# Performance work log

Measured on AMD Instinct MI355X. Metric: run time of the kernel, lower is better.

## Reference

```python
import jax, jax.numpy as jnp
import numpy as np

HIDDEN = 2048
NUM_EXPERTS = 64
TOP_K = 2


def setup_inputs() -> dict:
    key = jax.random.key(0)
    k1, k2 = jax.random.split(key)
    x = jax.random.normal(k1, (4, 4096, HIDDEN), dtype=jnp.float32)
    # nn.Linear(hidden, num_experts, bias=False): weight shape [E, H], y = x @ W.T
    W = jax.random.normal(k2, (NUM_EXPERTS, HIDDEN), dtype=jnp.float32) * (HIDDEN ** -0.5)
    return {"x": x, "W": W}


def reference(x, W):
    B, S, H = x.shape
    E, K = NUM_EXPERTS, TOP_K
    xf = x.reshape(-1, H)                       # [N, H]
    gate_logits = xf @ W.T                      # [N, E]
    routing_probs = jax.nn.softmax(gate_logits, axis=-1)
    top_k_probs, top_k_indices = jax.lax.top_k(routing_probs, K)  # [N, K]
    denom = jnp.sum(top_k_probs, axis=-1, keepdims=True) + 1e-6
    routing_weights = (top_k_probs / denom).reshape(B, S, K)
    expert_indices = top_k_indices.reshape(B, S, K)

    # aux load-balancing loss (training path)
    N = xf.shape[0]
    # expert_mask.mean(0): fraction of tokens assigned to each expert
    assign_per_expert = jnp.zeros((E,), jnp.float32).at[top_k_indices.reshape(-1)].add(1.0) / N
    prob_per_expert = jnp.mean(routing_probs, axis=0)             # [E]
    aux_loss = (jnp.sum(prob_per_expert * prob_per_expert) * E
                + jnp.sum(assign_per_expert * assign_per_expert) * E)

    # expert_counts update (bincount over selected indices)
    expert_counts = jnp.zeros((E,), jnp.float32).at[top_k_indices.reshape(-1)].add(1.0)

    return routing_weights, expert_indices, aux_loss, expert_counts
```

## Files before the change

kernel.cpp:

```cpp
#include <hip/hip_runtime.h>

#define HID 2048
#define NEXP 64
#define NTOK 16384
#define TM 32
#define NTHREADS 256
#define NBLK (NTOK / TM)
#define NCHUNK 32
#define KPH 4
#define CPW 8
#define CHUNK_B 24576
#define WS_W_OFF 262144

#define OUT_IDX_OFF (2 * NTOK)
#define OUT_AUX_OFF (4 * NTOK)
#define OUT_CNT_OFF (4 * NTOK + 1)

typedef __attribute__((ext_vector_type(8))) short bhalf8;
typedef __attribute__((ext_vector_type(16))) float f32x16;

__device__ __forceinline__ void split3(float v, unsigned short& h1, unsigned short& h2, unsigned short& h3) {
    unsigned int u = __float_as_uint(v);
    unsigned int r1 = (u + 0x7FFFu + ((u >> 16) & 1u)) & 0xFFFF0000u;
    float f1 = __uint_as_float(r1);
    float d1 = v - f1;
    unsigned int u2 = __float_as_uint(d1);
    unsigned int r2 = (u2 + 0x7FFFu + ((u2 >> 16) & 1u)) & 0xFFFF0000u;
    float f2 = __uint_as_float(r2);
    float d2 = d1 - f2;
    h1 = (unsigned short)(r1 >> 16);
    h2 = (unsigned short)(r2 >> 16);
    h3 = (unsigned short)(__float_as_uint(d2) >> 16);
}

__device__ __forceinline__ void xsplit(float4 va, float4 vb, bhalf8& o1, bhalf8& o2, bhalf8& o3) {
    float f[8] = {va.x, va.y, va.z, va.w, vb.x, vb.y, vb.z, vb.w};
    union U { bhalf8 v; unsigned int u[4]; } u1, u2, u3;
#pragma unroll
    for (int t = 0; t < 4; t++) {
        float a = f[2 * t], b = f[2 * t + 1];
        unsigned int ua = __float_as_uint(a), ub = __float_as_uint(b);
        float da = a - __uint_as_float(ua & 0xFFFF0000u);
        float db = b - __uint_as_float(ub & 0xFFFF0000u);
        unsigned int uda = __float_as_uint(da), udb = __float_as_uint(db);
        float da2 = da - __uint_as_float(uda & 0xFFFF0000u);
        float db2 = db - __uint_as_float(udb & 0xFFFF0000u);
        u1.u[t] = (ua >> 16) | (ub & 0xFFFF0000u);
        u2.u[t] = (uda >> 16) | (udb & 0xFFFF0000u);
        u3.u[t] = (__float_as_uint(da2) >> 16) | (__float_as_uint(db2) & 0xFFFF0000u);
    }
    o1 = u1.v; o2 = u2.v; o3 = u3.v;
}

__global__ __launch_bounds__(256) void wsplit_kernel(const float* __restrict__ W,
                                                     char* __restrict__ wq) {
    int idx8 = (blockIdx.x * 256 + threadIdx.x) * 8;
    int e = idx8 >> 11;
    int k0 = idx8 & 2047;
    int c = k0 >> 6, ks = (k0 >> 4) & 3, half = (k0 >> 3) & 1;
    int g = e >> 5, l = (e & 31) + 32 * half;
    const float4* wp = (const float4*)(W + (size_t)e * HID + k0);
    float4 v0 = wp[0], v1 = wp[1];
    float f[8] = {v0.x, v0.y, v0.z, v0.w, v1.x, v1.y, v1.z, v1.w};
    unsigned int p1[4], p2[4], p3[4];
#pragma unroll
    for (int t = 0; t < 4; t++) {
        unsigned short a1, a2, a3, b1, b2, b3;
        split3(f[2 * t], a1, a2, a3);
        split3(f[2 * t + 1], b1, b2, b3);
        p1[t] = (unsigned int)a1 | ((unsigned int)b1 << 16);
        p2[t] = (unsigned int)a2 | ((unsigned int)b2 << 16);
        p3[t] = (unsigned int)a3 | ((unsigned int)b3 << 16);
    }
    char* base = wq + (size_t)(((c * 4 + ks) * 3 + 0) * 2 + g) * 1024 + l * 16;
    *(uint4*)(base)        = make_uint4(p1[0], p1[1], p1[2], p1[3]);
    *(uint4*)(base + 2048) = make_uint4(p2[0], p2[1], p2[2], p2[3]);
    *(uint4*)(base + 4096) = make_uint4(p3[0], p3[1], p3[2], p3[3]);
}

__device__ __forceinline__ void load_chunk(const float* xc, float4 (&pa)[4], float4 (&pb)[4]) {
#pragma unroll
    for (int ks = 0; ks < 4; ks++) {
        pa[ks] = *(const float4*)(xc + ks * 16);
        pb[ks] = *(const float4*)(xc + ks * 16 + 4);
    }
}

__device__ __forceinline__ void compute_chunk(const float4 (&pa)[4], const float4 (&pb)[4],
                                              const char* wc, f32x16& acc0, f32x16& acc1) {
#pragma unroll
    for (int ks = 0; ks < 4; ks++) {
        bhalf8 A1, A2, A3;
        xsplit(pa[ks], pb[ks], A1, A2, A3);
        const char* wk = wc + ks * 6144;
        bhalf8 B1 = *(const bhalf8*)(wk);
        bhalf8 B2 = *(const bhalf8*)(wk + 2048);
        bhalf8 B3 = *(const bhalf8*)(wk + 4096);
        acc0 = __builtin_amdgcn_mfma_f32_32x32x16_bf16(A1, B1, acc0, 0, 0, 0);
        acc0 = __builtin_amdgcn_mfma_f32_32x32x16_bf16(A1, B2, acc0, 0, 0, 0);
        acc0 = __builtin_amdgcn_mfma_f32_32x32x16_bf16(A2, B1, acc0, 0, 0, 0);
        acc0 = __builtin_amdgcn_mfma_f32_32x32x16_bf16(A1, B3, acc0, 0, 0, 0);
        acc0 = __builtin_amdgcn_mfma_f32_32x32x16_bf16(A2, B2, acc0, 0, 0, 0);
        acc0 = __builtin_amdgcn_mfma_f32_32x32x16_bf16(A3, B1, acc0, 0, 0, 0);
        bhalf8 C1 = *(const bhalf8*)(wk + 1024);
        bhalf8 C2 = *(const bhalf8*)(wk + 2048 + 1024);
        bhalf8 C3 = *(const bhalf8*)(wk + 4096 + 1024);
        acc1 = __builtin_amdgcn_mfma_f32_32x32x16_bf16(A1, C1, acc1, 0, 0, 0);
        acc1 = __builtin_amdgcn_mfma_f32_32x32x16_bf16(A1, C2, acc1, 0, 0, 0);
        acc1 = __builtin_amdgcn_mfma_f32_32x32x16_bf16(A2, C1, acc1, 0, 0, 0);
        acc1 = __builtin_amdgcn_mfma_f32_32x32x16_bf16(A1, C3, acc1, 0, 0, 0);
        acc1 = __builtin_amdgcn_mfma_f32_32x32x16_bf16(A2, C2, acc1, 0, 0, 0);
        acc1 = __builtin_amdgcn_mfma_f32_32x32x16_bf16(A3, C1, acc1, 0, 0, 0);
    }
}

__global__ __launch_bounds__(NTHREADS, 2) void router_main(
    const float* __restrict__ x, const char* __restrict__ wq,
    float* __restrict__ out, float* __restrict__ partials)
{
    __shared__ float slab[KPH * TM * 68];
    __shared__ float smax[TM];
    __shared__ float sinvZ[TM];
    __shared__ float scount[NEXP];
    __shared__ float sprob[NEXP];

    const int tid = threadIdx.x;
    const int w = tid >> 6;
    const int lane = tid & 63;
    const int r = lane & 31;
    const int h = lane >> 5;
    const int n0 = blockIdx.x * TM;

    const float* xrow = x + (size_t)(n0 + r) * HID + h * 8;

    f32x16 acc0, acc1;
#pragma unroll
    for (int i = 0; i < 16; i++) { acc0[i] = 0.f; acc1[i] = 0.f; }

    float4 pa0[4], pb0[4], pa1[4], pb1[4];
    const float* xbase = xrow + (w * CPW) * 64;
    load_chunk(xbase, pa0, pb0);
    const char* wcbase = wq + (size_t)(w * CPW) * CHUNK_B + lane * 16;

#pragma unroll 1
    for (int i = 0; i < CPW; i += 2) {
        if (i + 1 < CPW) load_chunk(xbase + (i + 1) * 64, pa1, pb1);
        compute_chunk(pa0, pb0, wcbase + (size_t)i * CHUNK_B, acc0, acc1);
        if (i + 2 < CPW) load_chunk(xbase + (i + 2) * 64, pa0, pb0);
        if (i + 1 < CPW) compute_chunk(pa1, pb1, wcbase + (size_t)(i + 1) * CHUNK_B, acc0, acc1);
    }

#pragma unroll
    for (int reg = 0; reg < 16; reg++) {
        int row = (reg & 3) + 8 * (reg >> 2) + 4 * h;
        slab[(w * TM + row) * 68 + r]      = acc0[reg];
        slab[(w * TM + row) * 68 + 32 + r] = acc1[reg];
    }
    if (tid < NEXP) { scount[tid] = 0.f; sprob[tid] = 0.f; }
    __syncthreads();

    float* logits = slab;
#pragma unroll
    for (int idx = tid; idx < TM * NEXP; idx += NTHREADS) {
        int t = idx >> 6, e = idx & 63;
        logits[t * 68 + e] = slab[(0 * TM + t) * 68 + e] + slab[(1 * TM + t) * 68 + e]
                           + slab[(2 * TM + t) * 68 + e] + slab[(3 * TM + t) * 68 + e];
    }
    __syncthreads();

    if (tid < TM) {
        const int t = tid;
        float m1 = -3.4e38f, m2 = -3.4e38f;
        int i1 = 0, i2 = 0;
        for (int e = 0; e < NEXP; e++) {
            float v = logits[t * 68 + e];
            if (v > m1) { m2 = m1; i2 = i1; m1 = v; i1 = e; }
            else if (v > m2) { m2 = v; i2 = e; }
        }
        float Z = 0.f;
        for (int e = 0; e < NEXP; e++)
            Z += __expf(logits[t * 68 + e] - m1);
        float invZ = 1.f / Z;
        float p1 = invZ;
        float p2 = __expf(m2 - m1) * invZ;
        float denom = p1 + p2 + 1e-6f;
        int n = n0 + t;
        out[2 * n + 0] = p1 / denom;
        out[2 * n + 1] = p2 / denom;
        out[OUT_IDX_OFF + 2 * n + 0] = (float)i1;
        out[OUT_IDX_OFF + 2 * n + 1] = (float)i2;
        smax[t] = m1;
        sinvZ[t] = invZ;
        atomicAdd(&scount[i1], 1.f);
        atomicAdd(&scount[i2], 1.f);
    }
    __syncthreads();

    {
        const int e = tid & 63, tq = tid >> 6;
        float s = 0.f;
#pragma unroll
        for (int j = 0; j < 8; j++) {
            int t = tq * 8 + j;
            s += __expf(logits[t * 68 + e] - smax[t]) * sinvZ[t];
        }
        atomicAdd(&sprob[e], s);
    }
    __syncthreads();

    if (tid < NEXP) {
        partials[blockIdx.x * 128 + tid]      = sprob[tid];
        partials[blockIdx.x * 128 + 64 + tid] = scount[tid];
    }
}

__global__ __launch_bounds__(128) void router_finish(const float* __restrict__ partials,
                                                     float* __restrict__ out)
{
    __shared__ float red[2];
    const int t = threadIdx.x;
    float s = 0.f;
#pragma unroll 8
    for (int b = 0; b < NBLK; b++)
        s += partials[b * 128 + t];
    const float invN = 1.f / (float)NTOK;
    if (t >= 64) out[OUT_CNT_OFF + (t - 64)] = s;
    float sc = s * invN;
    float v = sc * sc;
#pragma unroll
    for (int off = 32; off > 0; off >>= 1)
        v += __shfl_down(v, off);
    if ((t & 63) == 0) red[t >> 6] = v;
    __syncthreads();
    if (t == 0) out[OUT_AUX_OFF] = (red[0] + red[1]) * (float)NEXP;
}

extern "C" void kernel_launch(void* const* d_in, const int* in_sizes, int n_in,
                              void* d_out, int out_size, void* d_ws, size_t ws_size,
                              hipStream_t stream)
{
    const float* x = (const float*)d_in[0];
    const float* W = (const float*)d_in[1];
    float* out = (float*)d_out;
    float* partials = (float*)d_ws;
    char* wq = (char*)d_ws + WS_W_OFF;

    wsplit_kernel<<<64, 256, 0, stream>>>(W, wq);
    router_main<<<NBLK, NTHREADS, 0, stream>>>(x, wq, out, partials);
    router_finish<<<1, 128, 0, stream>>>(partials, out);
}
```

Baseline: 229.9 us.

## Split router GEMM across token and expert tiles with 16x16 MFMA

Replaces the K-split work division, where each of 4 waves covered a quarter of the hidden dimension over all 32 tokens and 64 experts, with an output-tile split. Each of 8 waves now owns 16 tokens by 16 experts over the full hidden dimension, using 16x16x32 bf16 MFMA and a matching new weight layout. This removes the cross-wave slab reduction in shared memory and doubles the threads per block. The finish kernel also spreads the partial reduction over 1024 threads. The cost is that x rows are now read by four waves each, so global or cache traffic for x rises.

Measured after the change: 262.3 us. +14.1%, slower.

```diff
diff --git a/kernel.cpp b/kernel.cpp
--- a/kernel.cpp
+++ b/kernel.cpp
@@ -4,12 +4,9 @@
 #define NEXP 64
 #define NTOK 16384
 #define TM 32
-#define NTHREADS 256
+#define NTHREADS 512
 #define NBLK (NTOK / TM)
-#define NCHUNK 32
-#define KPH 4
-#define CPW 8
-#define CHUNK_B 24576
+#define NKS 64
 #define WS_W_OFF 262144
 
 #define OUT_IDX_OFF (2 * NTOK)
@@ -17,7 +14,7 @@
 #define OUT_CNT_OFF (4 * NTOK + 1)
 
 typedef __attribute__((ext_vector_type(8))) short bhalf8;
-typedef __attribute__((ext_vector_type(16))) float f32x16;
+typedef __attribute__((ext_vector_type(4))) float f32x4;
 
 __device__ __forceinline__ void split3(float v, unsigned short& h1, unsigned short& h2, unsigned short& h3) {
     unsigned int u = __float_as_uint(v);
@@ -57,8 +54,8 @@
     int idx8 = (blockIdx.x * 256 + threadIdx.x) * 8;
     int e = idx8 >> 11;
     int k0 = idx8 & 2047;
-    int c = k0 >> 6, ks = (k0 >> 4) & 3, half = (k0 >> 3) & 1;
-    int g = e >> 5, l = (e & 31) + 32 * half;
+    int ks = k0 >> 5, q = (k0 >> 3) & 3;
+    int eh = e >> 4, lane = q * 16 + (e & 15);
     const float4* wp = (const float4*)(W + (size_t)e * HID + k0);
     float4 v0 = wp[0], v1 = wp[1];
     float f[8] = {v0.x, v0.y, v0.z, v0.w, v1.x, v1.y, v1.z, v1.w};
@@ -72,53 +69,31 @@
         p2[t] = (unsigned int)a2 | ((unsigned int)b2 << 16);
         p3[t] = (unsigned int)a3 | ((unsigned int)b3 << 16);
     }
-    char* base = wq + (size_t)(((c * 4 + ks) * 3 + 0) * 2 + g) * 1024 + l * 16;
+    char* base = wq + (size_t)((ks * 3 + 0) * 4 + eh) * 1024 + lane * 16;
     *(uint4*)(base)        = make_uint4(p1[0], p1[1], p1[2], p1[3]);
-    *(uint4*)(base + 2048) = make_uint4(p2[0], p2[1], p2[2], p2[3]);
-    *(uint4*)(base + 4096) = make_uint4(p3[0], p3[1], p3[2], p3[3]);
-}
-
-__device__ __forceinline__ void load_chunk(const float* xc, float4 (&pa)[4], float4 (&pb)[4]) {
-#pragma unroll
-    for (int ks = 0; ks < 4; ks++) {
-        pa[ks] = *(const float4*)(xc + ks * 16);
-        pb[ks] = *(const float4*)(xc + ks * 16 + 4);
-    }
-}
-
-__device__ __forceinline__ void compute_chunk(const float4 (&pa)[4], const float4 (&pb)[4],
-                                              const char* wc, f32x16& acc0, f32x16& acc1) {
-#pragma unroll
-    for (int ks = 0; ks < 4; ks++) {
-        bhalf8 A1, A2, A3;
-        xsplit(pa[ks], pb[ks], A1, A2, A3);
-        const char* wk = wc + ks * 6144;
-        bhalf8 B1 = *(const bhalf8*)(wk);
-        bhalf8 B2 = *(const bhalf8*)(wk + 2048);
-        bhalf8 B3 = *(const bhalf8*)(wk + 4096);
-        acc0 = __builtin_amdgcn_mfma_f32_32x32x16_bf16(A1, B1, acc0, 0, 0, 0);
-        acc0 = __builtin_amdgcn_mfma_f32_32x32x16_bf16(A1, B2, acc0, 0, 0, 0);
-        acc0 = __builtin_amdgcn_mfma_f32_32x32x16_bf16(A2, B1, acc0, 0, 0, 0);
-        acc0 = __builtin_amdgcn_mfma_f32_32x32x16_bf16(A1, B3, acc0, 0, 0, 0);
-        acc0 = __builtin_amdgcn_mfma_f32_32x32x16_bf16(A2, B2, acc0, 0, 0, 0);
-        acc0 = __builtin_amdgcn_mfma_f32_32x32x16_bf16(A3, B1, acc0, 0, 0, 0);
-        bhalf8 C1 = *(const bhalf8*)(wk + 1024);
-        bhalf8 C2 = *(const bhalf8*)(wk + 2048 + 1024);
-        bhalf8 C3 = *(const bhalf8*)(wk + 4096 + 1024);
-        acc1 = __builtin_amdgcn_mfma_f32_32x32x16_bf16(A1, C1, acc1, 0, 0, 0);
-        acc1 = __builtin_amdgcn_mfma_f32_32x32x16_bf16(A1, C2, acc1, 0, 0, 0);
-        acc1 = __builtin_amdgcn_mfma_f32_32x32x16_bf16(A2, C1, acc1, 0, 0, 0);
-        acc1 = __builtin_amdgcn_mfma_f32_32x32x16_bf16(A1, C3, acc1, 0, 0, 0);
-        acc1 = __builtin_amdgcn_mfma_f32_32x32x16_bf16(A2, C2, acc1, 0, 0, 0);
-        acc1 = __builtin_amdgcn_mfma_f32_32x32x16_bf16(A3, C1, acc1, 0, 0, 0);
-    }
-}
-
-__global__ __launch_bounds__(NTHREADS, 2) void router_main(
+    *(uint4*)(base + 4096) = make_uint4(p2[0], p2[1], p2[2], p2[3]);
+    *(uint4*)(base + 8192) = make_uint4(p3[0], p3[1], p3[2], p3[3]);
+}
+
+__device__ __forceinline__ void kstep6(float4 xa, float4 xb, const char* wk, f32x4& acc) {
+    bhalf8 A1, A2, A3;
+    xsplit(xa, xb, A1, A2, A3);
+    bhalf8 B1 = *(const bhalf8*)(wk);
+    bhalf8 B2 = *(const bhalf8*)(wk + 4096);
+    bhalf8 B3 = *(const bhalf8*)(wk + 8192);
+    acc = __builtin_amdgcn_mfma_f32_16x16x32_bf16(A1, B1, acc, 0, 0, 0);
+    acc = __builtin_amdgcn_mfma_f32_16x16x32_bf16(A1, B2, acc, 0, 0, 0);
+    acc = __builtin_amdgcn_mfma_f32_16x16x32_bf16(A2, B1, acc, 0, 0, 0);
+    acc = __builtin_amdgcn_mfma_f32_16x16x32_bf16(A1, B3, acc, 0, 0, 0);
+    acc = __builtin_amdgcn_mfma_f32_16x16x32_bf16(A2, B2, acc, 0, 0, 0);
+    acc = __builtin_amdgcn_mfma_f32_16x16x32_bf16(A3, B1, acc, 0, 0, 0);
+}
+
+__global__ __launch_bounds__(NTHREADS, 4) void router_main(
     const float* __restrict__ x, const char* __restrict__ wq,
     float* __restrict__ out, float* __restrict__ partials)
 {
-    __shared__ float slab[KPH * TM * 68];
+    __shared__ float logits[TM * 68];
     __shared__ float smax[TM];
     __shared__ float sinvZ[TM];
     __shared__ float scount[NEXP];
@@ -127,45 +102,41 @@
     const int tid = threadIdx.x;
     const int w = tid >> 6;
     const int lane = tid & 63;
-    const int r = lane & 31;
-    const int h = lane >> 5;
+    const int th = w >> 2;
+    const int eh = w & 3;
+    const int m = lane & 15;
+    const int q = lane >> 4;
     const int n0 = blockIdx.x * TM;
 
-    const float* xrow = x + (size_t)(n0 + r) * HID + h * 8;
-
-    f32x16 acc0, acc1;
-#pragma unroll
-    for (int i = 0; i < 16; i++) { acc0[i] = 0.f; acc1[i] = 0.f; }
-
-    float4 pa0[4], pb0[4], pa1[4], pb1[4];
-    const float* xbase = xrow + (w * CPW) * 64;
-    load_chunk(xbase, pa0, pb0);
-    const char* wcbase = wq + (size_t)(w * CPW) * CHUNK_B + lane * 16;
+    const float* xrow = x + (size_t)(n0 + th * 16 + m) * HID + q * 8;
+    const char* wbase = wq + (size_t)eh * 1024 + lane * 16;
+
+    f32x4 accA = {0.f, 0.f, 0.f, 0.f}, accB = {0.f, 0.f, 0.f, 0.f};
+
+    float4 xa0 = *(const float4*)(xrow);
+    float4 xb0 = *(const float4*)(xrow + 4);
+    float4 xa1 = *(const float4*)(xrow + 32);
+    float4 xb1 = *(const float4*)(xrow + 36);
 
 #pragma unroll 1
-    for (int i = 0; i < CPW; i += 2) {
-        if (i + 1 < CPW) load_chunk(xbase + (i + 1) * 64, pa1, pb1);
-        compute_chunk(pa0, pb0, wcbase + (size_t)i * CHUNK_B, acc0, acc1);
-        if (i + 2 < CPW) load_chunk(xbase + (i + 2) * 64, pa0, pb0);
-        if (i + 1 < CPW) compute_chunk(pa1, pb1, wcbase + (size_t)(i + 1) * CHUNK_B, acc0, acc1);
-    }
-
-#pragma unroll
-    for (int reg = 0; reg < 16; reg++) {
-        int row = (reg & 3) + 8 * (reg >> 2) + 4 * h;
-        slab[(w * TM + row) * 68 + r]      = acc0[reg];
-        slab[(w * TM + row) * 68 + 32 + r] = acc1[reg];
-    }
+    for (int ks = 0; ks < NKS; ks += 2) {
+        float4 ya, yb, za, zb;
+        if (ks + 2 < NKS) {
+            const float* xn = xrow + (ks + 2) * 32;
+            ya = *(const float4*)(xn);
+            yb = *(const float4*)(xn + 4);
+            za = *(const float4*)(xn + 32);
+            zb = *(const float4*)(xn + 36);
+        }
+        kstep6(xa0, xb0, wbase + (size_t)ks * 12288, accA);
+        kstep6(xa1, xb1, wbase + (size_t)(ks + 1) * 12288, accB);
+        xa0 = ya; xb0 = yb; xa1 = za; xb1 = zb;
+    }
+
+#pragma unroll
+    for (int r = 0; r < 4; r++)
+        logits[(th * 16 + q * 4 + r) * 68 + eh * 16 + m] = accA[r] + accB[r];
     if (tid < NEXP) { scount[tid] = 0.f; sprob[tid] = 0.f; }
-    __syncthreads();
-
-    float* logits = slab;
-#pragma unroll
-    for (int idx = tid; idx < TM * NEXP; idx += NTHREADS) {
-        int t = idx >> 6, e = idx & 63;
-        logits[t * 68 + e] = slab[(0 * TM + t) * 68 + e] + slab[(1 * TM + t) * 68 + e]
-                           + slab[(2 * TM + t) * 68 + e] + slab[(3 * TM + t) * 68 + e];
-    }
     __syncthreads();
 
     if (tid < TM) {
@@ -200,8 +171,8 @@
         const int e = tid & 63, tq = tid >> 6;
         float s = 0.f;
 #pragma unroll
-        for (int j = 0; j < 8; j++) {
-            int t = tq * 8 + j;
+        for (int j = 0; j < 4; j++) {
+            int t = tq * 4 + j;
             s += __expf(logits[t * 68 + e] - smax[t]) * sinvZ[t];
         }
         atomicAdd(&sprob[e], s);
@@ -214,25 +185,33 @@
     }
 }
 
-__global__ __launch_bounds__(128) void router_finish(const float* __restrict__ partials,
-                                                     float* __restrict__ out)
+__global__ __launch_bounds__(1024) void router_finish(const float* __restrict__ partials,
+                                                      float* __restrict__ out)
 {
+    __shared__ float sred[8 * 128];
     __shared__ float red[2];
-    const int t = threadIdx.x;
+    const int t = threadIdx.x & 127;
+    const int g = threadIdx.x >> 7;
     float s = 0.f;
 #pragma unroll 8
-    for (int b = 0; b < NBLK; b++)
-        s += partials[b * 128 + t];
-    const float invN = 1.f / (float)NTOK;
-    if (t >= 64) out[OUT_CNT_OFF + (t - 64)] = s;
-    float sc = s * invN;
-    float v = sc * sc;
-#pragma unroll
-    for (int off = 32; off > 0; off >>= 1)
-        v += __shfl_down(v, off);
-    if ((t & 63) == 0) red[t >> 6] = v;
-    __syncthreads();
-    if (t == 0) out[OUT_AUX_OFF] = (red[0] + red[1]) * (float)NEXP;
+    for (int i = 0; i < 64; i++)
+        s += partials[(g * 64 + i) * 128 + t];
+    sred[g * 128 + t] = s;
+    __syncthreads();
+    if (threadIdx.x < 128) {
+        float tot = 0.f;
+#pragma unroll
+        for (int gg = 0; gg < 8; gg++) tot += sred[gg * 128 + t];
+        if (t >= 64) out[OUT_CNT_OFF + (t - 64)] = tot;
+        float sc = tot * (1.f / (float)NTOK);
+        float v = sc * sc;
+#pragma unroll
+        for (int off = 32; off > 0; off >>= 1)
+            v += __shfl_down(v, off);
+        if ((t & 63) == 0) red[t >> 6] = v;
+    }
+    __syncthreads();
+    if (threadIdx.x == 0) out[OUT_AUX_OFF] = (red[0] + red[1]) * (float)NEXP;
 }
 
 extern "C" void kernel_launch(void* const* d_in, const int* in_sizes, int n_in,
@@ -247,5 +226,5 @@
 
     wsplit_kernel<<<64, 256, 0, stream>>>(W, wq);
     router_main<<<NBLK, NTHREADS, 0, stream>>>(x, wq, out, partials);
-    router_finish<<<1, 128, 0, stream>>>(partials, out);
-}
+    router_finish<<<1, 1024, 0, stream>>>(partials, out);
+}
```

## Double waves per block, rotate chunk order across blocks, parallelize final reduction

Applied to the files above, without the earlier changes.

The main kernel now runs 8 waves per 512-thread block, splitting the hidden dimension into 8 partial sums of 4 chunks each instead of 4 waves with 8 chunks each. Chunk order is rotated by block index so concurrent blocks read different parts of the weight buffer, and the unrolled-by-two prefetch is replaced by a single-step prefetch with register copies. The finish kernel uses 1024 threads to reduce the 512 block partials in 8 parallel groups, which shortens its serial loop. The costs are larger slab shared memory (8x32x68 floats), higher occupancy demands from the launch bounds (4 blocks of 512 threads), and possible register pressure.

New measurement: 243.7 us. 6.0% more time.

```diff
diff --git a/kernel.cpp b/kernel.cpp
--- a/kernel.cpp
+++ b/kernel.cpp
@@ -4,11 +4,11 @@
 #define NEXP 64
 #define NTOK 16384
 #define TM 32
-#define NTHREADS 256
+#define NTHREADS 512
 #define NBLK (NTOK / TM)
 #define NCHUNK 32
-#define KPH 4
-#define CPW 8
+#define KPH 8
+#define CPW 4
 #define CHUNK_B 24576
 #define WS_W_OFF 262144
 
@@ -114,7 +114,7 @@
     }
 }
 
-__global__ __launch_bounds__(NTHREADS, 2) void router_main(
+__global__ __launch_bounds__(NTHREADS, 4) void router_main(
     const float* __restrict__ x, const char* __restrict__ wq,
     float* __restrict__ out, float* __restrict__ partials)
 {
@@ -130,6 +130,7 @@
     const int r = lane & 31;
     const int h = lane >> 5;
     const int n0 = blockIdx.x * TM;
+    const int brot = blockIdx.x & 3;
 
     const float* xrow = x + (size_t)(n0 + r) * HID + h * 8;
 
@@ -138,16 +139,17 @@
     for (int i = 0; i < 16; i++) { acc0[i] = 0.f; acc1[i] = 0.f; }
 
     float4 pa0[4], pb0[4], pa1[4], pb1[4];
-    const float* xbase = xrow + (w * CPW) * 64;
-    load_chunk(xbase, pa0, pb0);
-    const char* wcbase = wq + (size_t)(w * CPW) * CHUNK_B + lane * 16;
+    int c0 = w + 8 * brot;
+    load_chunk(xrow + c0 * 64, pa0, pb0);
 
 #pragma unroll 1
-    for (int i = 0; i < CPW; i += 2) {
-        if (i + 1 < CPW) load_chunk(xbase + (i + 1) * 64, pa1, pb1);
-        compute_chunk(pa0, pb0, wcbase + (size_t)i * CHUNK_B, acc0, acc1);
-        if (i + 2 < CPW) load_chunk(xbase + (i + 2) * 64, pa0, pb0);
-        if (i + 1 < CPW) compute_chunk(pa1, pb1, wcbase + (size_t)(i + 1) * CHUNK_B, acc0, acc1);
+    for (int i = 0; i < CPW; i++) {
+        int cn = w + 8 * ((i + 1 + brot) & 3);
+        if (i + 1 < CPW) load_chunk(xrow + cn * 64, pa1, pb1);
+        int c = w + 8 * ((i + brot) & 3);
+        compute_chunk(pa0, pb0, wq + (size_t)c * CHUNK_B + lane * 16, acc0, acc1);
+#pragma unroll
+        for (int ks = 0; ks < 4; ks++) { pa0[ks] = pa1[ks]; pb0[ks] = pb1[ks]; }
     }
 
 #pragma unroll
@@ -163,8 +165,10 @@
 #pragma unroll
     for (int idx = tid; idx < TM * NEXP; idx += NTHREADS) {
         int t = idx >> 6, e = idx & 63;
-        logits[t * 68 + e] = slab[(0 * TM + t) * 68 + e] + slab[(1 * TM + t) * 68 + e]
-                           + slab[(2 * TM + t) * 68 + e] + slab[(3 * TM + t) * 68 + e];
+        float v = 0.f;
+#pragma unroll
+        for (int p = 0; p < KPH; p++) v += slab[(p * TM + t) * 68 + e];
+        logits[t * 68 + e] = v;
     }
     __syncthreads();
 
@@ -200,39 +204,47 @@
         const int e = tid & 63, tq = tid >> 6;
         float s = 0.f;
 #pragma unroll
-        for (int j = 0; j < 8; j++) {
-            int t = tq * 8 + j;
+        for (int j = 0; j < 4; j++) {
+            int t = tq * 4 + j;
             s += __expf(logits[t * 68 + e] - smax[t]) * sinvZ[t];
         }
         atomicAdd(&sprob[e], s);
     }
     __syncthreads();
 
-    if (tid < NEXP) {
-        partials[blockIdx.x * 128 + tid]      = sprob[tid];
-        partials[blockIdx.x * 128 + 64 + tid] = scount[tid];
-    }
-}
-
-__global__ __launch_bounds__(128) void router_finish(const float* __restrict__ partials,
-                                                     float* __restrict__ out)
+    if (tid < 128) {
+        float v = (tid < 64) ? sprob[tid] : scount[tid - 64];
+        partials[blockIdx.x * 128 + tid] = v;
+    }
+}
+
+__global__ __launch_bounds__(1024) void router_finish(const float* __restrict__ partials,
+                                                      float* __restrict__ out)
 {
+    __shared__ float sred[8 * 128];
     __shared__ float red[2];
-    const int t = threadIdx.x;
+    const int t = threadIdx.x & 127;
+    const int g = threadIdx.x >> 7;
     float s = 0.f;
 #pragma unroll 8
-    for (int b = 0; b < NBLK; b++)
-        s += partials[b * 128 + t];
-    const float invN = 1.f / (float)NTOK;
-    if (t >= 64) out[OUT_CNT_OFF + (t - 64)] = s;
-    float sc = s * invN;
-    float v = sc * sc;
-#pragma unroll
-    for (int off = 32; off > 0; off >>= 1)
-        v += __shfl_down(v, off);
-    if ((t & 63) == 0) red[t >> 6] = v;
-    __syncthreads();
-    if (t == 0) out[OUT_AUX_OFF] = (red[0] + red[1]) * (float)NEXP;
+    for (int i = 0; i < 64; i++)
+        s += partials[(g * 64 + i) * 128 + t];
+    sred[g * 128 + t] = s;
+    __syncthreads();
+    if (threadIdx.x < 128) {
+        float tot = 0.f;
+#pragma unroll
+        for (int gg = 0; gg < 8; gg++) tot += sred[gg * 128 + t];
+        if (t >= 64) out[OUT_CNT_OFF + (t - 64)] = tot;
+        float sc = tot * (1.f / (float)NTOK);
+        float v = sc * sc;
+#pragma unroll
+        for (int off = 32; off > 0; off >>= 1)
+            v += __shfl_down(v, off);
+        if ((t & 63) == 0) red[t >> 6] = v;
+    }
+    __syncthreads();
+    if (threadIdx.x == 0) out[OUT_AUX_OFF] = (red[0] + red[1]) * (float)NEXP;
 }
 
 extern "C" void kernel_launch(void* const* d_in, const int* in_sizes, int n_in,
@@ -247,5 +259,5 @@
 
     wsplit_kernel<<<64, 256, 0, stream>>>(W, wq);
     router_main<<<NBLK, NTHREADS, 0, stream>>>(x, wq, out, partials);
-    router_finish<<<1, 128, 0, stream>>>(partials, out);
-}
+    router_finish<<<1, 1024, 0, stream>>>(partials, out);
+}
```
